# Kernel tuning notes

Measured on AMD Instinct MI355X. Metric: run time of the kernel, lower is better.

Reference implementation:

```python
import jax, jax.numpy as jnp
import numpy as np

USR_NUM = 100000
D_IN = 32
D_HID = 32
D_MID = 16
D_OUT = 2
N_EDGES = 1600000
EPS = 1e-16  # matches torch_geometric.utils.softmax denominator eps


def _glorot(key, shape):
    fan_in, fan_out = shape[0], shape[1]
    lim = np.sqrt(6.0 / (fan_in + fan_out))
    return jax.random.uniform(key, shape, jnp.float32, -lim, lim)


def setup_inputs() -> dict:
    key = jax.random.key(0)
    ks = jax.random.split(key, 16)
    inp = {
        "edge_index": jax.random.randint(ks[0], (2, N_EDGES), 0, USR_NUM, dtype=jnp.int64)
        if jax.config.jax_enable_x64 else jax.random.randint(ks[0], (2, N_EDGES), 0, USR_NUM).astype(jnp.int32),
        "emb": jax.random.normal(ks[1], (USR_NUM, D_IN), jnp.float32),
        # conv1: TransformerConv(32 -> 32, heads=1)
        "Wq1": _glorot(ks[2], (D_IN, D_HID)), "bq1": jnp.zeros((D_HID,), jnp.float32),
        "Wk1": _glorot(ks[3], (D_IN, D_HID)), "bk1": jnp.zeros((D_HID,), jnp.float32),
        "Wv1": _glorot(ks[4], (D_IN, D_HID)), "bv1": jnp.zeros((D_HID,), jnp.float32),
        "Ws1": _glorot(ks[5], (D_IN, D_HID)), "bs1": jnp.zeros((D_HID,), jnp.float32),
        # conv2: TransformerConv(32 -> 16, heads=1)
        "Wq2": _glorot(ks[6], (D_HID, D_MID)), "bq2": jnp.zeros((D_MID,), jnp.float32),
        "Wk2": _glorot(ks[7], (D_HID, D_MID)), "bk2": jnp.zeros((D_MID,), jnp.float32),
        "Wv2": _glorot(ks[8], (D_HID, D_MID)), "bv2": jnp.zeros((D_MID,), jnp.float32),
        "Ws2": _glorot(ks[9], (D_HID, D_MID)), "bs2": jnp.zeros((D_MID,), jnp.float32),
        # output: Linear(16 -> 2)
        "Wo": _glorot(ks[10], (D_MID, D_OUT)), "bo": jnp.zeros((D_OUT,), jnp.float32),
    }
    return inp


def transformer_conv(x, src, dst, Wq, bq, Wk, bk, Wv, bv, Ws, bs, n_nodes):
    # edge (j=src -> i=dst): alpha_ij = softmax_i( <q_i, k_j> / sqrt(d) )
    d = Wq.shape[1]
    q = (x @ Wq + bq)[dst]          # [E, d]
    k = (x @ Wk + bk)[src]          # [E, d]
    v = (x @ Wv + bv)[src]          # [E, d]
    alpha = jnp.sum(q * k, axis=-1) / jnp.sqrt(jnp.float32(d))  # [E]
    # segment softmax over incoming edges of each destination node
    seg_max = jax.ops.segment_max(alpha, dst, num_segments=n_nodes)  # [N]
    e = jnp.exp(alpha - seg_max[dst])
    seg_sum = jax.ops.segment_sum(e, dst, num_segments=n_nodes)      # [N]
    w = e / (seg_sum[dst] + EPS)
    agg = jax.ops.segment_sum(v * w[:, None], dst, num_segments=n_nodes)  # [N, d]
    return agg + x @ Ws + bs  # root/skip connection (PyG default root_weight=True)


def reference(edge_index, emb,
              Wq1, bq1, Wk1, bk1, Wv1, bv1, Ws1, bs1,
              Wq2, bq2, Wk2, bk2, Wv2, bv2, Ws2, bs2,
              Wo, bo):
    src, dst = edge_index[0], edge_index[1]
    h = transformer_conv(emb, src, dst, Wq1, bq1, Wk1, bk1, Wv1, bv1, Ws1, bs1, USR_NUM)
    h = jax.nn.relu(h)
    h = transformer_conv(h, src, dst, Wq2, bq2, Wk2, bk2, Wv2, bv2, Ws2, bs2, USR_NUM)
    h = jax.nn.relu(h)
    return h @ Wo + bo  # [N, 2]
```

## Files before the change

kernel.cpp:

```cpp
#include <hip/hip_runtime.h>
#include <hip/hip_bf16.h>

typedef __hip_bfloat16 bf16;
typedef unsigned int uint;
typedef unsigned short ushort;

#define N_NODES 100000
#define N_EDGES_C 1600000
#define NSB2 1568
#define NSB2P 1792
#define RND 2048
#define EPB (RND / 256)
#define NBIN 64
#define G_RAD ((N_EDGES_C + RND - 1) / RND)
#define HCAP 1536
#define NSLOT (NSB2 * 64)
#define NCHUNK 8
#define KEYN (64 * NCHUNK)

__device__ __forceinline__ float ldf(const void* p, long i, int isbf) {
    return isbf ? __bfloat162float(((const bf16*)p)[i]) : ((const float*)p)[i];
}
__device__ __forceinline__ int ldidx(const int* ei, long pos, int is64) {
    return is64 ? ei[2 * pos] : ei[pos];
}
__device__ __forceinline__ ushort bfb(float x) {
    bf16 h = __float2bfloat16(x);
    return *(ushort*)&h;
}
__device__ __forceinline__ float bl(uint u) { return __uint_as_float(u << 16); }
__device__ __forceinline__ float bh(uint u) { return __uint_as_float(u & 0xFFFF0000u); }

struct BuildS { int dcnt[KEYN]; int dexcl[KEYN]; int hbin[NBIN]; int hbase[NBIN]; int hcur[NBIN]; };

__device__ __forceinline__ void build_csr(
    int sbh, int n, const uint* __restrict__ srcp,
    BuildS* b, int* sEsrc, int* sRB, int* sRE, int* sPerm) {
    int t = threadIdx.x;
    for (int i = t; i < KEYN; i += 256) b->dcnt[i] = 0;
    if (t < NBIN) { b->hbin[t] = 0; b->hcur[t] = 0; }
    if (t < 64) sPerm[t] = -1;
    __syncthreads();
    for (int i = t; i < n; i += 256) {
        uint pk = srcp[i];
        int key = (int)((pk >> 17) & 63) * NCHUNK + (int)((pk & 0x1FFFFu) >> 14);
        atomicAdd(&b->dcnt[key], 1);
    }
    __syncthreads();
    int mybin = -1;
    if (t < 64) {
        const int kb = t * NCHUNK;
        int sum = 0;
#pragma unroll
        for (int j = 0; j < NCHUNK; j++) sum += b->dcnt[kb + j];
        int v = sum;
        int x = v;
#pragma unroll
        for (int off = 1; off < 64; off <<= 1) {
            int u2 = __shfl_up(x, off, 64);
            if (t >= off) x += u2;
        }
        int myExcl = x - v;
        int run = myExcl;
#pragma unroll
        for (int j = 0; j < NCHUNK; j++) { b->dexcl[kb + j] = run; run += b->dcnt[kb + j]; }
        sRB[t] = myExcl;
        sRE[t] = myExcl + v;
        int dst = sbh * 64 + t;
        if (dst < N_NODES) {
            mybin = min(v, NBIN - 1);
            atomicAdd(&b->hbin[mybin], 1);
        }
    }
    __syncthreads();
    if (t < 64) {
        int hv = b->hbin[t];
        int sfx = hv;
#pragma unroll
        for (int off = 1; off < 64; off <<= 1) {
            int u2 = __shfl_down(sfx, off, 64);
            if (t + off < 64) sfx += u2;
        }
        b->hbase[t] = sfx - hv;
    }
    __syncthreads();
    if (t < 64 && mybin >= 0) {
        int r = atomicAdd(&b->hcur[mybin], 1);
        sPerm[b->hbase[mybin] + r] = t;
    }
    for (int i = t; i < n; i += 256) {
        uint pk = srcp[i];
        int key = (int)((pk >> 17) & 63) * NCHUNK + (int)((pk & 0x1FFFFu) >> 14);
        int p2 = atomicAdd(&b->dexcl[key], 1);
        sEsrc[p2] = (int)(pk & 0x1FFFF);
    }
    __syncthreads();
}

__global__ void setup_kernel(
    const void* emb, const int* ei,
    const void* Wq1, const void* bq1, const void* Wk1, const void* bk1,
    const void* Wv1, const void* bv1, const void* Ws1, const void* bs1,
    const void* Wq2, const void* bq2, const void* Wk2, const void* bk2,
    const void* Wv2, const void* bv2, const void* Ws2, const void* bs2,
    const void* Wo, const void* bo,
    int* flags, float* wp1, float* bp1, float* wp2, float* bp2, float* woF,
    int* curSB) {
    __shared__ int sf0;
    int t = threadIdx.x;
    if (t < 64) {
        const bf16* pb = (const bf16*)emb;
        int bad = 0;
        for (int i = t; i < 256; i += 64) {
            float v = __bfloat162float(pb[i]);
            if (!(v > -1.0e6f && v < 1.0e6f)) bad++;
        }
        int nz = 0;
        for (int i = 2 * t + 1; i < 256; i += 128) nz += (ei[i] != 0) ? 1 : 0;
#pragma unroll
        for (int m = 32; m >= 1; m >>= 1) {
            bad += __shfl_xor(bad, m, 64);
            nz  += __shfl_xor(nz, m, 64);
        }
        if (t == 0) {
            int f0 = (bad <= 8) ? 1 : 0;
            flags[0] = f0;
            flags[1] = (nz == 0) ? 1 : 0;
            sf0 = f0;
        }
    }
    __syncthreads();
    int isbf = sf0;
    for (int i = t; i < 1024; i += 256) {
        wp1[i]        = ldf(Wq1, i, isbf);
        wp1[1024 + i] = ldf(Wk1, i, isbf);
        wp1[2048 + i] = ldf(Wv1, i, isbf);
        wp1[3072 + i] = ldf(Ws1, i, isbf);
    }
    for (int i = t; i < 512; i += 256) {
        wp2[i]        = ldf(Wq2, i, isbf);
        wp2[512 + i]  = ldf(Wk2, i, isbf);
        wp2[1024 + i] = ldf(Wv2, i, isbf);
        wp2[1536 + i] = ldf(Ws2, i, isbf);
    }
    if (t < 32) {
        bp1[t] = ldf(bq1, t, isbf); bp1[32 + t] = ldf(bk1, t, isbf);
        bp1[64 + t] = ldf(bv1, t, isbf); bp1[96 + t] = ldf(bs1, t, isbf);
        woF[t] = ldf(Wo, t, isbf);
    }
    if (t < 16) {
        bp2[t] = ldf(bq2, t, isbf); bp2[16 + t] = ldf(bk2, t, isbf);
        bp2[32 + t] = ldf(bv2, t, isbf); bp2[48 + t] = ldf(bs2, t, isbf);
    }
    if (t < 2) woF[32 + t] = ldf(bo, t, isbf);
    for (int i = t; i < NSB2P; i += 256) curSB[i] = 0;
}

template <int DOUT, bool RUNTIME_DTYPE>
__device__ __forceinline__ void node_linear_body(
    const void* __restrict__ X, const float* __restrict__ wpack,
    const float* __restrict__ bpack, const int* __restrict__ flags,
    float* __restrict__ q, ushort* __restrict__ kvb, float* __restrict__ s,
    int bid, float* __restrict__ sW, float* __restrict__ sbias, float* __restrict__ sX) {
    const int TPN = DOUT / 4;
    const int NPB = 256 / TPN;
    const int W_ELEMS = 4 * 32 * DOUT;

    const float4* wp4 = (const float4*)wpack;
    float4* sW4 = (float4*)sW;
    for (int i = threadIdx.x; i < W_ELEMS / 4; i += 256) sW4[i] = wp4[i];
    if (threadIdx.x < 4 * DOUT) sbias[threadIdx.x] = bpack[threadIdx.x];
    const int base = bid * NPB * 32;
    bool useBf = RUNTIME_DTYPE && (flags[0] != 0);
    if (useBf) {
        for (int i = threadIdx.x; i < NPB * 32; i += 256) {
            int g = base + i;
            float xv = (g < N_NODES * 32) ? __bfloat162float(((const bf16*)X)[g]) : 0.0f;
            sX[(i >> 5) * 36 + (i & 31)] = xv;
        }
    } else {
        for (int i = threadIdx.x; i < NPB * 32; i += 256) {
            int g = base + i;
            sX[(i >> 5) * 36 + (i & 31)] = (g < N_NODES * 32) ? ((const float*)X)[g] : 0.0f;
        }
    }
    __syncthreads();

    int l = threadIdx.x / TPN;
    int c4 = (threadIdx.x % TPN) * 4;
    int n = bid * NPB + l;
    if (n >= N_NODES) return;

    float xr[32];
#pragma unroll
    for (int j = 0; j < 8; j++) {
        float4 t4 = *(const float4*)&sX[l * 36 + 4 * j];
        xr[4 * j] = t4.x; xr[4 * j + 1] = t4.y; xr[4 * j + 2] = t4.z; xr[4 * j + 3] = t4.w;
    }
    float acc[4][4];
#pragma unroll
    for (int m = 0; m < 4; m++)
#pragma unroll
        for (int j = 0; j < 4; j++) acc[m][j] = sbias[m * DOUT + c4 + j];

#pragma unroll
    for (int t = 0; t < 32; t++) {
#pragma unroll
        for (int m = 0; m < 4; m++) {
            float4 w = *(const float4*)&sW[(m * 32 + t) * DOUT + c4];
            acc[m][0] += xr[t] * w.x;
            acc[m][1] += xr[t] * w.y;
            acc[m][2] += xr[t] * w.z;
            acc[m][3] += xr[t] * w.w;
        }
    }
    size_t o = (size_t)n * DOUT + c4;
    *(float4*)&q[o] = make_float4(acc[0][0], acc[0][1], acc[0][2], acc[0][3]);
    *(float4*)&s[o] = make_float4(acc[3][0], acc[3][1], acc[3][2], acc[3][3]);
    size_t okv = (size_t)n * 2 * DOUT + c4;
    ushort4 kp = make_ushort4(bfb(acc[1][0]), bfb(acc[1][1]), bfb(acc[1][2]), bfb(acc[1][3]));
    ushort4 vp = make_ushort4(bfb(acc[2][0]), bfb(acc[2][1]), bfb(acc[2][2]), bfb(acc[2][3]));
    *(ushort4*)&kvb[okv]        = kp;
    *(ushort4*)&kvb[okv + DOUT] = vp;
}

struct RadixS { int cnt[NSB2P]; int gbase[NSB2P]; };
struct LinS { float sW[4096]; float sbias[128]; float sX[32 * 36]; };
union alignas(16) FusedS { RadixS r; LinS l; };

__global__ void __launch_bounds__(256, 4) fused_ra_nl(
    const int* __restrict__ ei, const int* __restrict__ flags,
    int* __restrict__ curSB, uint* __restrict__ pairsSB,
    const void* __restrict__ X, const float* __restrict__ wpack,
    const float* __restrict__ bpack,
    float* __restrict__ q, ushort* __restrict__ kvb, float* __restrict__ s) {
    __shared__ FusedS u;
    if (blockIdx.x >= G_RAD) {
        node_linear_body<32, true>(X, wpack, bpack, flags, q, kvb, s,
                                   (int)blockIdx.x - G_RAD, u.l.sW, u.l.sbias, u.l.sX);
        return;
    }
    int* cnt = u.r.cnt; int* gbase = u.r.gbase;
    const int is64 = flags[1];
    int t = threadIdx.x;
    for (int i = t; i < NSB2P; i += 256) cnt[i] = 0;
    __syncthreads();
    long base = (long)blockIdx.x * RND;

    int mySb[EPB]; int myRank[EPB]; uint myPk[EPB];
#pragma unroll
    for (int r = 0; r < EPB; r++) {
        long e = base + r * 256 + t;
        mySb[r] = -1;
        if (e < N_EDGES_C) {
            int d = ldidx(ei, (long)N_EDGES_C + e, is64);
            int src = ldidx(ei, e, is64);
            int sb = d >> 6;
            myPk[r] = (uint)src | ((uint)(d & 63) << 17);
            myRank[r] = atomicAdd(&cnt[sb], 1);
            mySb[r] = sb;
        }
    }
    __syncthreads();
    for (int i = t; i < NSB2P; i += 256)
        gbase[i] = (cnt[i] > 0) ? atomicAdd(&curSB[i], cnt[i]) : 0;
    __syncthreads();
#pragma unroll
    for (int r = 0; r < EPB; r++) {
        if (mySb[r] >= 0) {
            int gp = gbase[mySb[r]] + myRank[r];
            if (gp < HCAP)
                pairsSB[(size_t)mySb[r] * HCAP + gp] = myPk[r];
        }
    }
}

__global__ void gather_attn_l1(const int* __restrict__ curSB, const uint* __restrict__ pairsSB,
                               const float* __restrict__ q, const ushort* __restrict__ kvb,
                               const float* __restrict__ s,
                               const float* __restrict__ wp2,
                               const float* __restrict__ bp2,
                               float* __restrict__ q2o, ushort* __restrict__ kvb2o,
                               float* __restrict__ s2o) {
    const int D = 32;
    const int LPD = 4;
    const int G = 16;
    __shared__ float sW2[2048];
    __shared__ float sb2[64];
    union GU { BuildS b; float sH[64 * 36]; };
    __shared__ GU gu;
    __shared__ int sEsrc[HCAP];
    __shared__ int sDst[64], sPerm[64], sRB[64], sRE[64];

    int sbh = blockIdx.x;
    int n = min(curSB[sbh], HCAP);
    for (int i = threadIdx.x; i < 2048; i += 256) sW2[i] = wp2[i];
    if (threadIdx.x < 64) sb2[threadIdx.x] = bp2[threadIdx.x];
    build_csr(sbh, n, pairsSB + (size_t)sbh * HCAP, &gu.b, sEsrc, sRB, sRE, sPerm);

    int lane = threadIdx.x & 63;
    int wave = threadIdx.x >> 6;
    int g = lane / LPD;
    int c = lane % LPD;
    int rank = wave * G + g;
    int dl = sPerm[rank];
    bool alive = (dl >= 0);
    int dst = sbh * 64 + dl;

    const float rsq = 0.17677669529663689f;
    float4 qa = make_float4(0.f, 0.f, 0.f, 0.f), qb = qa;
    int beg = 0, end = 0;
    if (alive) {
        qa = *(const float4*)(q + (size_t)dst * D + 8 * c);
        qb = *(const float4*)(q + (size_t)dst * D + 8 * c + 4);
        beg = sRB[dl]; end = sRE[dl];
    }

    const char* kvbase = (const char*)kvb;
    const int ROW = 4 * D;
    const int koff = 16 * c;
    const int voff = 2 * D + 16 * c;

    float sum0 = 0.f, sum1 = 0.f;
    float a0[8] = {0,0,0,0,0,0,0,0};
    float a1[8] = {0,0,0,0,0,0,0,0};

    uint4 kq[4], vq[4];
#pragma unroll
    for (int r = 0; r < 4; r++) {
        int sn = (beg + r < end) ? sEsrc[beg + r] : 0;
        const char* p = kvbase + (size_t)sn * ROW;
        kq[r] = *(const uint4*)(p + koff);
        vq[r] = *(const uint4*)(p + voff);
    }

    for (int e = beg; e < end; e += 4) {
        uint4 kc[4], vc[4];
#pragma unroll
        for (int r = 0; r < 4; r++) { kc[r] = kq[r]; vc[r] = vq[r]; }
#pragma unroll
        for (int r = 0; r < 4; r++) {
            if (e + 4 + r < end) {
                const char* p = kvbase + (size_t)sEsrc[e + 4 + r] * ROW;
                kq[r] = *(const uint4*)(p + koff);
                vq[r] = *(const uint4*)(p + voff);
            }
        }
#pragma unroll
        for (int r = 0; r < 4; r++) {
            if (e + r < end) {
                uint4 kA = kc[r], vA = vc[r];
                float pd = qa.x * bl(kA.x) + qa.y * bh(kA.x) + qa.z * bl(kA.y) + qa.w * bh(kA.y)
                         + qb.x * bl(kA.z) + qb.y * bh(kA.z) + qb.z * bl(kA.w) + qb.w * bh(kA.w);
#pragma unroll
                for (int m = LPD / 2; m >= 1; m >>= 1) pd += __shfl_xor(pd, m, LPD);
                float ex = __expf(fminf(fmaxf(pd * rsq, -80.0f), 80.0f));
                if (r & 1) {
                    sum1 += ex;
                    a1[0] += bl(vA.x) * ex; a1[1] += bh(vA.x) * ex;
                    a1[2] += bl(vA.y) * ex; a1[3] += bh(vA.y) * ex;
                    a1[4] += bl(vA.z) * ex; a1[5] += bh(vA.z) * ex;
                    a1[6] += bl(vA.w) * ex; a1[7] += bh(vA.w) * ex;
                } else {
                    sum0 += ex;
                    a0[0] += bl(vA.x) * ex; a0[1] += bh(vA.x) * ex;
                    a0[2] += bl(vA.y) * ex; a0[3] += bh(vA.y) * ex;
                    a0[4] += bl(vA.z) * ex; a0[5] += bh(vA.z) * ex;
                    a0[6] += bl(vA.w) * ex; a0[7] += bh(vA.w) * ex;
                }
            }
        }
    }
    float inv = 1.0f / (sum0 + sum1 + 1e-16f);
    float4 sa = make_float4(0.f, 0.f, 0.f, 0.f), sbv = sa;
    if (alive) {
        sa  = *(const float4*)(s + (size_t)dst * D + 8 * c);
        sbv = *(const float4*)(s + (size_t)dst * D + 8 * c + 4);
    }
    float h[8];
    h[0] = (a0[0] + a1[0]) * inv + sa.x;  h[1] = (a0[1] + a1[1]) * inv + sa.y;
    h[2] = (a0[2] + a1[2]) * inv + sa.z;  h[3] = (a0[3] + a1[3]) * inv + sa.w;
    h[4] = (a0[4] + a1[4]) * inv + sbv.x; h[5] = (a0[5] + a1[5]) * inv + sbv.y;
    h[6] = (a0[6] + a1[6]) * inv + sbv.z; h[7] = (a0[7] + a1[7]) * inv + sbv.w;
#pragma unroll
    for (int j = 0; j < 8; j++) h[j] = h[j] > 0.0f ? h[j] : 0.0f;

    int gl = wave * G + g;
    if (alive) {
        *(float4*)&gu.sH[gl * 36 + 8 * c]     = make_float4(h[0], h[1], h[2], h[3]);
        *(float4*)&gu.sH[gl * 36 + 8 * c + 4] = make_float4(h[4], h[5], h[6], h[7]);
    }
    if (c == 0) sDst[gl] = alive ? dst : -1;
    __syncthreads();
    int l = threadIdx.x >> 2;
    int c4 = (threadIdx.x & 3) * 4;
    int nd = sDst[l];
    if (nd >= 0) {
        float acc2[4][4];
#pragma unroll
        for (int m = 0; m < 4; m++)
#pragma unroll
            for (int j = 0; j < 4; j++) acc2[m][j] = sb2[m * 16 + c4 + j];
#pragma unroll
        for (int t2 = 0; t2 < 32; t2++) {
            float xv = gu.sH[l * 36 + t2];
#pragma unroll
            for (int m = 0; m < 4; m++) {
                float4 w = *(const float4*)&sW2[(m * 32 + t2) * 16 + c4];
                acc2[m][0] += xv * w.x;
                acc2[m][1] += xv * w.y;
                acc2[m][2] += xv * w.z;
                acc2[m][3] += xv * w.w;
            }
        }
        size_t o = (size_t)nd * 16 + c4;
        *(float4*)&q2o[o] = make_float4(acc2[0][0], acc2[0][1], acc2[0][2], acc2[0][3]);
        *(float4*)&s2o[o] = make_float4(acc2[3][0], acc2[3][1], acc2[3][2], acc2[3][3]);
        size_t okv = (size_t)nd * 32 + c4;
        ushort4 kp = make_ushort4(bfb(acc2[1][0]), bfb(acc2[1][1]), bfb(acc2[1][2]), bfb(acc2[1][3]));
        ushort4 vp = make_ushort4(bfb(acc2[2][0]), bfb(acc2[2][1]), bfb(acc2[2][2]), bfb(acc2[2][3]));
        *(ushort4*)&kvb2o[okv]      = kp;
        *(ushort4*)&kvb2o[okv + 16] = vp;
    }
}

__global__ void gather_attn_l2(const int* __restrict__ curSB, const uint* __restrict__ pairsSB,
                               const float* __restrict__ q, const ushort* __restrict__ kvb,
                               const float* __restrict__ s,
                               const float* __restrict__ woF,
                               const int* __restrict__ flags,
                               void* __restrict__ out) {
    const int D = 16;
    const int LG = 4;
    const int KL = 2;
    const int G  = 16;
    __shared__ BuildS bs;
    __shared__ int sEsrc[HCAP];
    __shared__ int sPerm[64], sRB[64], sRE[64];

    int sbh = blockIdx.x;
    int n = min(curSB[sbh], HCAP);
    build_csr(sbh, n, pairsSB + (size_t)sbh * HCAP, &bs, sEsrc, sRB, sRE, sPerm);

    int lane = threadIdx.x & 63;
    int wave = threadIdx.x >> 6;
    int g = lane / LG;
    int sub = lane % LG;
    bool isK = (sub < KL);
    int cv = sub - KL;
    int rank = wave * G + g;
    int dl = sPerm[rank];
    if (dl < 0) return;
    int dst = sbh * 64 + dl;

    const float rsq = 0.25f;
    float qacc[8] = {0,0,0,0,0,0,0,0};
    if (isK) {
        float4 qa = *(const float4*)(q + (size_t)dst * D + 8 * sub);
        float4 qb = *(const float4*)(q + (size_t)dst * D + 8 * sub + 4);
        qacc[0] = qa.x; qacc[1] = qa.y; qacc[2] = qa.z; qacc[3] = qa.w;
        qacc[4] = qb.x; qacc[5] = qb.y; qacc[6] = qb.z; qacc[7] = qb.w;
    }
    int beg = sRB[dl], end = sRE[dl];

    const char* kvbase = (const char*)kvb + 16 * sub;
    const int ROW = 4 * D;

    float sum = 0.f;

    uint4 rv[4];
    int sn1[4];
#pragma unroll
    for (int r = 0; r < 4; r++) {
        int sn = (beg + r < end) ? sEsrc[beg + r] : 0;
        rv[r] = *(const uint4*)(kvbase + (size_t)sn * ROW);
    }
#pragma unroll
    for (int r = 0; r < 4; r++)
        sn1[r] = (beg + 4 + r < end) ? sEsrc[beg + 4 + r] : 0;

    for (int e = beg; e < end; e += 4) {
        uint4 rc[4];
#pragma unroll
        for (int r = 0; r < 4; r++) rc[r] = rv[r];
#pragma unroll
        for (int r = 0; r < 4; r++) {
            if (e + 4 + r < end)
                rv[r] = *(const uint4*)(kvbase + (size_t)sn1[r] * ROW);
        }
#pragma unroll
        for (int r = 0; r < 4; r++) {
            if (e + 8 + r < end) sn1[r] = sEsrc[e + 8 + r];
        }
#pragma unroll
        for (int r = 0; r < 4; r++) {
            if (e + r < end) {
                uint4 rA = rc[r];
                float pd = 0.f;
                if (isK) {
                    pd = qacc[0] * bl(rA.x) + qacc[1] * bh(rA.x)
                       + qacc[2] * bl(rA.y) + qacc[3] * bh(rA.y)
                       + qacc[4] * bl(rA.z) + qacc[5] * bh(rA.z)
                       + qacc[6] * bl(rA.w) + qacc[7] * bh(rA.w);
                }
                pd += __shfl_xor(pd, 1, KL);
                float pdx = __shfl_xor(pd, KL, LG);
                float pdf = isK ? pd : pdx;
                float ex = __expf(fminf(fmaxf(pdf * rsq, -80.0f), 80.0f));
                sum += ex;
                if (!isK) {
                    qacc[0] += bl(rA.x) * ex; qacc[1] += bh(rA.x) * ex;
                    qacc[2] += bl(rA.y) * ex; qacc[3] += bh(rA.y) * ex;
                    qacc[4] += bl(rA.z) * ex; qacc[5] += bh(rA.z) * ex;
                    qacc[6] += bl(rA.w) * ex; qacc[7] += bh(rA.w) * ex;
                }
            }
        }
    }
    float inv = 1.0f / (sum + 1e-16f);
    float p0 = 0.f, p1 = 0.f;
    if (!isK) {
        float4 sa  = *(const float4*)(s + (size_t)dst * D + 8 * cv);
        float4 sbv = *(const float4*)(s + (size_t)dst * D + 8 * cv + 4);
        float h[8];
        h[0] = qacc[0] * inv + sa.x;  h[1] = qacc[1] * inv + sa.y;
        h[2] = qacc[2] * inv + sa.z;  h[3] = qacc[3] * inv + sa.w;
        h[4] = qacc[4] * inv + sbv.x; h[5] = qacc[5] * inv + sbv.y;
        h[6] = qacc[6] * inv + sbv.z; h[7] = qacc[7] * inv + sbv.w;
#pragma unroll
        for (int j = 0; j < 8; j++) h[j] = h[j] > 0.0f ? h[j] : 0.0f;
#pragma unroll
        for (int j = 0; j < 8; j++) {
            p0 += h[j] * woF[(8 * cv + j) * 2 + 0];
            p1 += h[j] * woF[(8 * cv + j) * 2 + 1];
        }
    }
    p0 += __shfl_xor(p0, 1, 2);
    p1 += __shfl_xor(p1, 1, 2);
    if (sub == KL) {
        float o0 = p0 + woF[32];
        float o1 = p1 + woF[33];
        if (flags[0]) {
            ((bf16*)out)[dst * 2 + 0] = __float2bfloat16(o0);
            ((bf16*)out)[dst * 2 + 1] = __float2bfloat16(o1);
        } else {
            ((float*)out)[dst * 2 + 0] = o0;
            ((float*)out)[dst * 2 + 1] = o1;
        }
    }
}

extern "C" void kernel_launch(void* const* d_in, const int* in_sizes, int n_in,
                              void* d_out, int out_size, void* d_ws, size_t ws_size,
                              hipStream_t stream) {
    const int* ei  = (const int*)d_in[0];
    const void* emb = d_in[1];
    const void *Wq1 = d_in[2],  *bq1 = d_in[3];
    const void *Wk1 = d_in[4],  *bk1 = d_in[5];
    const void *Wv1 = d_in[6],  *bv1 = d_in[7];
    const void *Ws1 = d_in[8],  *bs1 = d_in[9];
    const void *Wq2 = d_in[10], *bq2 = d_in[11];
    const void *Wk2 = d_in[12], *bk2 = d_in[13];
    const void *Wv2 = d_in[14], *bv2 = d_in[15];
    const void *Ws2 = d_in[16], *bs2 = d_in[17];
    const void *Wo  = d_in[18], *bo  = d_in[19];

    const size_t ND   = (size_t)N_NODES * 32;
    const size_t ND16 = (size_t)N_NODES * 16;
    const size_t SBTOT = (size_t)NSB2 * HCAP;
    float* base   = (float*)d_ws;
    int*   flags  = (int*)base;
    float* wp1    = base + 64;
    float* bp1    = wp1 + 4096;
    float* wp2    = bp1 + 128;
    float* bp2    = wp2 + 2048;
    float* woF    = bp2 + 64;
    int*   curSB  = (int*)(woF + 64);
    float* p      = (float*)(curSB + NSB2P);
    p = (float*)(((uintptr_t)p + 127) & ~(uintptr_t)127);
    float* q      = p; p += ND;
    float* s      = p; p += ND;
    ushort* kvb   = (ushort*)p; p += ND;
    float* q2     = p; p += ND16;
    float* s2     = p; p += ND16;
    ushort* kvb2  = (ushort*)p; p += ND16;
    uint*  pairsSB = (uint*)p;

    const int B = 256;
    const int gNL32  = (N_NODES + 31) / 32;
    const int gFused = G_RAD + gNL32;

    setup_kernel<<<1, B, 0, stream>>>(emb, ei,
        Wq1, bq1, Wk1, bk1, Wv1, bv1, Ws1, bs1,
        Wq2, bq2, Wk2, bk2, Wv2, bv2, Ws2, bs2, Wo, bo,
        flags, wp1, bp1, wp2, bp2, woF, curSB);

    fused_ra_nl<<<gFused, B, 0, stream>>>(ei, flags, curSB, pairsSB,
                                          emb, wp1, bp1, q, kvb, s);

    gather_attn_l1<<<NSB2, B, 0, stream>>>(
        curSB, pairsSB, q, kvb, s, wp2, bp2, q2, kvb2, s2);

    gather_attn_l2<<<NSB2, B, 0, stream>>>(
        curSB, pairsSB, q2, kvb2, s2, woF, flags, d_out);
}
```

Measured before the change: 241.9 us.

## Radix-scatter edges into coarser 256-node buckets via shared staging for coalesced writes

```diff
diff --git a/kernel.cpp b/kernel.cpp
--- a/kernel.cpp
+++ b/kernel.cpp
@@ -7,14 +7,15 @@
 
 #define N_NODES 100000
 #define N_EDGES_C 1600000
-#define NSB2 1568
-#define NSB2P 1792
+#define NSB 392
+#define NSBP 512
+#define SBCAP 5632
+#define NGB 1568
 #define RND 2048
 #define EPB (RND / 256)
 #define NBIN 64
 #define G_RAD ((N_EDGES_C + RND - 1) / RND)
 #define HCAP 1536
-#define NSLOT (NSB2 * 64)
 #define NCHUNK 8
 #define KEYN (64 * NCHUNK)
 
@@ -34,17 +35,20 @@
 struct BuildS { int dcnt[KEYN]; int dexcl[KEYN]; int hbin[NBIN]; int hbase[NBIN]; int hcur[NBIN]; };
 
 __device__ __forceinline__ void build_csr(
-    int sbh, int n, const uint* __restrict__ srcp,
+    int sbh, int np, const uint* __restrict__ srcp,
     BuildS* b, int* sEsrc, int* sRB, int* sRE, int* sPerm) {
     int t = threadIdx.x;
+    uint quarter = (uint)(sbh & 3);
     for (int i = t; i < KEYN; i += 256) b->dcnt[i] = 0;
     if (t < NBIN) { b->hbin[t] = 0; b->hcur[t] = 0; }
     if (t < 64) sPerm[t] = -1;
     __syncthreads();
-    for (int i = t; i < n; i += 256) {
+    for (int i = t; i < np; i += 256) {
         uint pk = srcp[i];
-        int key = (int)((pk >> 17) & 63) * NCHUNK + (int)((pk & 0x1FFFFu) >> 14);
-        atomicAdd(&b->dcnt[key], 1);
+        if (((pk >> 23) & 3u) == quarter) {
+            int key = (int)((pk >> 17) & 63) * NCHUNK + (int)((pk & 0x1FFFFu) >> 14);
+            atomicAdd(&b->dcnt[key], 1);
+        }
     }
     __syncthreads();
     int mybin = -1;
@@ -64,8 +68,8 @@
         int run = myExcl;
 #pragma unroll
         for (int j = 0; j < NCHUNK; j++) { b->dexcl[kb + j] = run; run += b->dcnt[kb + j]; }
-        sRB[t] = myExcl;
-        sRE[t] = myExcl + v;
+        sRB[t] = min(myExcl, HCAP);
+        sRE[t] = min(myExcl + v, HCAP);
         int dst = sbh * 64 + t;
         if (dst < N_NODES) {
             mybin = min(v, NBIN - 1);
@@ -88,11 +92,13 @@
         int r = atomicAdd(&b->hcur[mybin], 1);
         sPerm[b->hbase[mybin] + r] = t;
     }
-    for (int i = t; i < n; i += 256) {
+    for (int i = t; i < np; i += 256) {
         uint pk = srcp[i];
-        int key = (int)((pk >> 17) & 63) * NCHUNK + (int)((pk & 0x1FFFFu) >> 14);
-        int p2 = atomicAdd(&b->dexcl[key], 1);
-        sEsrc[p2] = (int)(pk & 0x1FFFF);
+        if (((pk >> 23) & 3u) == quarter) {
+            int key = (int)((pk >> 17) & 63) * NCHUNK + (int)((pk & 0x1FFFFu) >> 14);
+            int p2 = atomicAdd(&b->dexcl[key], 1);
+            if (p2 < HCAP) sEsrc[p2] = (int)(pk & 0x1FFFF);
+        }
     }
     __syncthreads();
 }
@@ -153,7 +159,7 @@
         bp2[32 + t] = ldf(bv2, t, isbf); bp2[48 + t] = ldf(bs2, t, isbf);
     }
     if (t < 2) woF[32 + t] = ldf(bo, t, isbf);
-    for (int i = t; i < NSB2P; i += 256) curSB[i] = 0;
+    curSB[t] = 0; curSB[t + 256] = 0;
 }
 
 template <int DOUT, bool RUNTIME_DTYPE>
@@ -224,7 +230,10 @@
     *(ushort4*)&kvb[okv + DOUT] = vp;
 }
 
-struct RadixS { int cnt[NSB2P]; int gbase[NSB2P]; };
+struct RadixS {
+    int cnt[NSBP]; int excl[NSBP]; int gbase[NSBP]; int wsum[4];
+    uint sVal[RND]; ushort sSb[RND];
+};
 struct LinS { float sW[4096]; float sbias[128]; float sX[32 * 36]; };
 union alignas(16) FusedS { RadixS r; LinS l; };
 
@@ -240,10 +249,11 @@
                                    (int)blockIdx.x - G_RAD, u.l.sW, u.l.sbias, u.l.sX);
         return;
     }
-    int* cnt = u.r.cnt; int* gbase = u.r.gbase;
+    int* cnt = u.r.cnt; int* excl = u.r.excl; int* gbase = u.r.gbase;
+    uint* sVal = u.r.sVal; ushort* sSb = u.r.sSb;
     const int is64 = flags[1];
     int t = threadIdx.x;
-    for (int i = t; i < NSB2P; i += 256) cnt[i] = 0;
+    cnt[t] = 0; cnt[t + 256] = 0;
     __syncthreads();
     long base = (long)blockIdx.x * RND;
 
@@ -255,23 +265,48 @@
         if (e < N_EDGES_C) {
             int d = ldidx(ei, (long)N_EDGES_C + e, is64);
             int src = ldidx(ei, e, is64);
-            int sb = d >> 6;
-            myPk[r] = (uint)src | ((uint)(d & 63) << 17);
+            int sb = d >> 8;
+            myPk[r] = (uint)src | ((uint)(d & 255) << 17);
             myRank[r] = atomicAdd(&cnt[sb], 1);
             mySb[r] = sb;
         }
     }
     __syncthreads();
-    for (int i = t; i < NSB2P; i += 256)
-        gbase[i] = (cnt[i] > 0) ? atomicAdd(&curSB[i], cnt[i]) : 0;
+    int v0 = cnt[2 * t], v1 = cnt[2 * t + 1];
+    int sum2 = v0 + v1;
+    int lane6 = t & 63, wid6 = t >> 6;
+    int x = sum2;
+#pragma unroll
+    for (int off = 1; off < 64; off <<= 1) {
+        int u2 = __shfl_up(x, off, 64);
+        if (lane6 >= off) x += u2;
+    }
+    if (lane6 == 63) u.r.wsum[wid6] = x;
+    __syncthreads();
+    int wbase = 0;
+#pragma unroll
+    for (int w = 0; w < 4; w++) if (w < wid6) wbase += u.r.wsum[w];
+    int basex = wbase + x - sum2;
+    excl[2 * t]     = basex;
+    excl[2 * t + 1] = basex + v0;
     __syncthreads();
 #pragma unroll
     for (int r = 0; r < EPB; r++) {
         if (mySb[r] >= 0) {
-            int gp = gbase[mySb[r]] + myRank[r];
-            if (gp < HCAP)
-                pairsSB[(size_t)mySb[r] * HCAP + gp] = myPk[r];
-        }
+            int pos = excl[mySb[r]] + myRank[r];
+            sVal[pos] = myPk[r];
+            sSb[pos] = (ushort)mySb[r];
+        }
+    }
+    for (int i = t; i < NSBP; i += 256)
+        gbase[i] = (cnt[i] > 0) ? atomicAdd(&curSB[i], cnt[i]) : 0;
+    __syncthreads();
+    int tot = excl[NSBP - 1] + cnt[NSBP - 1];
+    for (int i = t; i < tot; i += 256) {
+        int sb = sSb[i];
+        int gp = gbase[sb] + (i - excl[sb]);
+        if (gp < SBCAP)
+            pairsSB[(size_t)sb * SBCAP + gp] = sVal[i];
     }
 }
 
@@ -293,10 +328,11 @@
     __shared__ int sDst[64], sPerm[64], sRB[64], sRE[64];
 
     int sbh = blockIdx.x;
-    int n = min(curSB[sbh], HCAP);
+    int parent = sbh >> 2;
+    int np = min(curSB[parent], SBCAP);
     for (int i = threadIdx.x; i < 2048; i += 256) sW2[i] = wp2[i];
     if (threadIdx.x < 64) sb2[threadIdx.x] = bp2[threadIdx.x];
-    build_csr(sbh, n, pairsSB + (size_t)sbh * HCAP, &gu.b, sEsrc, sRB, sRE, sPerm);
+    build_csr(sbh, np, pairsSB + (size_t)parent * SBCAP, &gu.b, sEsrc, sRB, sRE, sPerm);
 
     int lane = threadIdx.x & 63;
     int wave = threadIdx.x >> 6;
@@ -439,8 +475,9 @@
     __shared__ int sPerm[64], sRB[64], sRE[64];
 
     int sbh = blockIdx.x;
-    int n = min(curSB[sbh], HCAP);
-    build_csr(sbh, n, pairsSB + (size_t)sbh * HCAP, &bs, sEsrc, sRB, sRE, sPerm);
+    int parent = sbh >> 2;
+    int np = min(curSB[parent], SBCAP);
+    build_csr(sbh, np, pairsSB + (size_t)parent * SBCAP, &bs, sEsrc, sRB, sRE, sPerm);
 
     int lane = threadIdx.x & 63;
     int wave = threadIdx.x >> 6;
@@ -567,7 +604,7 @@
 
     const size_t ND   = (size_t)N_NODES * 32;
     const size_t ND16 = (size_t)N_NODES * 16;
-    const size_t SBTOT = (size_t)NSB2 * HCAP;
+    const size_t SBTOT = (size_t)NSB * SBCAP;
     float* base   = (float*)d_ws;
     int*   flags  = (int*)base;
     float* wp1    = base + 64;
@@ -576,7 +613,7 @@
     float* bp2    = wp2 + 2048;
     float* woF    = bp2 + 64;
     int*   curSB  = (int*)(woF + 64);
-    float* p      = (float*)(curSB + NSB2P);
+    float* p      = (float*)(curSB + NSBP);
     p = (float*)(((uintptr_t)p + 127) & ~(uintptr_t)127);
     float* q      = p; p += ND;
     float* s      = p; p += ND;
@@ -598,9 +635,9 @@
     fused_ra_nl<<<gFused, B, 0, stream>>>(ei, flags, curSB, pairsSB,
                                           emb, wp1, bp1, q, kvb, s);
 
-    gather_attn_l1<<<NSB2, B, 0, stream>>>(
+    gather_attn_l1<<<NGB, B, 0, stream>>>(
         curSB, pairsSB, q, kvb, s, wp2, bp2, q2, kvb2, s2);
 
-    gather_attn_l2<<<NSB2, B, 0, stream>>>(
+    gather_attn_l2<<<NGB, B, 0, stream>>>(
         curSB, pairsSB, q2, kvb2, s2, woF, flags, d_out);
 }
```

New measurement: 250.7 us. 1.04x slower.
